# Kernel optimization log

Hardware: AMD Instinct MI355X
Metric: run time of the kernel (lower is better)

The kernel has to match this reference:

```python
import jax, jax.numpy as jnp
import numpy as np
from jax import lax

NUM_HEADS = 8
EPS_BN = 1e-5
EPS_LN = 1e-5


def setup_inputs() -> dict:
    key = jax.random.key(0)
    ks = iter(jax.random.split(key, 32))
    C = 512
    R = C // 16  # channel-gate reduction
    HID = 512    # classifier hidden
    NC = 1       # num_classes

    def gn(shape, scale=0.02):
        return (jax.random.normal(next(ks), shape, dtype=jnp.float32) * scale)

    inp = {
        "x": jax.random.normal(next(ks), (16, C, 28, 28), dtype=jnp.float32),
        # ChannelGate MLP (Linear(C,R) -> ReLU -> Linear(R,C))
        "mlp_w1": gn((R, C)), "mlp_b1": jnp.zeros((R,), jnp.float32),
        "mlp_w2": gn((C, R)), "mlp_b2": jnp.zeros((C,), jnp.float32),
        # SpatialGate 7x7 conv (2->1, no bias) + BatchNorm2d(1) eval-mode stats
        "sp_w": gn((1, 2, 7, 7)),
        "sp_gamma": jnp.ones((1,), jnp.float32), "sp_beta": jnp.zeros((1,), jnp.float32),
        "sp_mean": jnp.zeros((1,), jnp.float32), "sp_var": jnp.ones((1,), jnp.float32),
        # attention projections
        "wq": gn((C, C)), "bq": jnp.zeros((C,), jnp.float32),
        "wk": gn((C, C)), "bk": jnp.zeros((C,), jnp.float32),
        "wv": gn((C, C)), "bv": jnp.zeros((C,), jnp.float32),
        "wo": gn((C, C)), "bo": jnp.zeros((C,), jnp.float32),
        # classifier: LayerNorm(C) -> Linear(C,512) -> ReLU -> Linear(512,NC)
        "ln_g": jnp.ones((C,), jnp.float32), "ln_b": jnp.zeros((C,), jnp.float32),
        "fc1_w": gn((HID, C)), "fc1_b": jnp.zeros((HID,), jnp.float32),
        "fc2_w": gn((NC, HID)), "fc2_b": jnp.zeros((NC,), jnp.float32),
    }
    return inp


def reference(x, mlp_w1, mlp_b1, mlp_w2, mlp_b2, sp_w, sp_gamma, sp_beta,
              sp_mean, sp_var, wq, bq, wk, bk, wv, bv, wo, bo,
              ln_g, ln_b, fc1_w, fc1_b, fc2_w, fc2_b):
    B, C, H, W = x.shape
    N = H * W
    hd = C // NUM_HEADS

    # ---- CBAM: channel gate (avg + max global pools through shared MLP) ----
    def mlp(p):  # p: [B, C]
        return jax.nn.relu(p @ mlp_w1.T + mlp_b1) @ mlp_w2.T + mlp_b2

    avg_p = x.mean(axis=(2, 3))
    max_p = x.max(axis=(2, 3))
    ch_scale = jax.nn.sigmoid(mlp(avg_p) + mlp(max_p))[:, :, None, None]
    x = x * ch_scale

    # ---- CBAM: spatial gate ----
    comp = jnp.concatenate([x.max(axis=1, keepdims=True),
                            x.mean(axis=1, keepdims=True)], axis=1)  # [B,2,H,W]
    s = lax.conv_general_dilated(comp, sp_w, window_strides=(1, 1),
                                 padding=[(3, 3), (3, 3)],
                                 dimension_numbers=("NCHW", "OIHW", "NCHW"))
    s = (s - sp_mean[None, :, None, None]) * lax.rsqrt(sp_var + EPS_BN)[None, :, None, None]
    s = s * sp_gamma[None, :, None, None] + sp_beta[None, :, None, None]
    x = x * jax.nn.sigmoid(s)

    # ---- multi-head self-attention over HW tokens ----
    xf = x.reshape(B, C, N).transpose(0, 2, 1)  # [B, N, C]

    def heads(w, b):
        return (xf @ w.T + b).reshape(B, N, NUM_HEADS, hd).transpose(0, 2, 1, 3)

    Q, K, V = heads(wq, bq), heads(wk, bk), heads(wv, bv)  # [B, h, N, d]
    scores = jnp.einsum("bhnd,bhmd->bhnm", Q, K) / jnp.sqrt(jnp.float32(hd))
    attn = jax.nn.softmax(scores, axis=-1)  # dropout is identity in eval
    attended = jnp.einsum("bhnm,bhmd->bhnd", attn, V)
    attended = attended.transpose(0, 2, 1, 3).reshape(B, N, C)
    attended = attended @ wo.T + bo
    x = x + attended.transpose(0, 2, 1).reshape(B, C, H, W)

    # ---- classifier head ----
    p = x.mean(axis=(2, 3))  # AdaptiveAvgPool2d(1) + Flatten -> [B, C]
    mu = p.mean(axis=-1, keepdims=True)
    var = p.var(axis=-1, keepdims=True)
    ln = (p - mu) * lax.rsqrt(var + EPS_LN) * ln_g + ln_b
    h = jax.nn.relu(ln @ fc1_w.T + fc1_b)
    return h @ fc2_w.T + fc2_b
```

## Files before the change

### kernel.cpp

```cpp
#include <hip/hip_runtime.h>
#include <math.h>

#define BB 16
#define CC 512
#define HW 784
#define RR 32
#define NHD 8
#define HD 64
#define NT 784
#define NTILE 49
#define CBS 132

#define OFS_AVGP   0
#define OFS_MAXP   8192
#define OFS_CHS    16384
#define OFS_SP     49664
#define OFS_P1     62208
#define OFS_ABAR   70400
#define OFS_XG     78592
#define XG_SZ      (BB*CC*HW)
#define OFS_XGT    (OFS_XG + XG_SZ)
#define OFS_QBF    (OFS_XGT + XG_SZ/2)
#define OFS_KBF    (OFS_QBF + XG_SZ/2)
#define OFS_V2     (OFS_KBF + XG_SZ/2)
#define OFS_WF     (OFS_V2 + XG_SZ)
#define OFS_W      OFS_XG
#define OFS_PV     (OFS_XG + 131072)
#define OFS_H1     (OFS_PV + 8192)
#define OFS_CMAXP  (OFS_XG + 262144)
#define OFS_CMEANP (OFS_CMAXP + 200704)

typedef __attribute__((ext_vector_type(8))) short bf16x8;
typedef __attribute__((ext_vector_type(4))) float f32x4;

__device__ __forceinline__ unsigned short f2bf(float x) {
  union { float f; unsigned u; } v; v.f = x;
  unsigned r = v.u + 0x7fffu + ((v.u >> 16) & 1u);
  return (unsigned short)(r >> 16);
}
__device__ __forceinline__ float bf2f(unsigned short x) {
  union { unsigned u; float f; } v; v.u = ((unsigned)x) << 16;
  return v.f;
}
__device__ __forceinline__ void async16(const unsigned short* g, unsigned short* l) {
  __builtin_amdgcn_global_load_lds(
      (const __attribute__((address_space(1))) unsigned int*)g,
      (__attribute__((address_space(3))) unsigned int*)l, 16, 0, 0);
}

__global__ void k_pool(const float* __restrict__ x, float* avg_p, float* max_p) {
  int wid = threadIdx.x >> 6;
  int lane = threadIdx.x & 63;
  int row = blockIdx.x * 4 + wid;
  const float* xr = x + (size_t)row * HW;
  float s = 0.f, m = -INFINITY;
  for (int i = lane; i < HW; i += 64) { float v = xr[i]; s += v; m = fmaxf(m, v); }
  for (int o = 32; o; o >>= 1) { s += __shfl_down(s, o, 64); m = fmaxf(m, __shfl_down(m, o, 64)); }
  if (lane == 0) { avg_p[row] = s * (1.f/HW); max_p[row] = m; }
}

__global__ void k_chmlp(const float* avg_p, const float* max_p,
                        const float* w1, const float* b1,
                        const float* w2, const float* b2, float* chs) {
  __shared__ float pa[CC], pm[CC], part[256], hr[64];
  int b = blockIdx.x, t = threadIdx.x;
  for (int i = t; i < CC; i += 256) { pa[i] = avg_p[b*CC+i]; pm[i] = max_p[b*CC+i]; }
  __syncthreads();
  {
    int rp = t & 63, ch = t >> 6;
    int r = rp & 31;
    const float* src = (rp < 32) ? pa : pm;
    const float* wr = w1 + (size_t)r*CC + ch*128;
    float s = 0.f;
    #pragma unroll 8
    for (int c = 0; c < 128; c++) s += src[ch*128 + c] * wr[c];
    part[t] = s;
  }
  __syncthreads();
  if (t < 64)
    hr[t] = fmaxf(part[t] + part[64+t] + part[128+t] + part[192+t] + b1[t & 31], 0.f);
  __syncthreads();
  for (int c = t; c < CC; c += 256) {
    float a = 2.f*b2[c];
    const float* wr = w2 + c*RR;
    #pragma unroll
    for (int r = 0; r < RR; r++) a += (hr[r]+hr[32+r])*wr[r];
    chs[b*CC+c] = 1.f/(1.f+__expf(-a));
  }
}

__global__ void k_chgatep(const float* __restrict__ x, const float* __restrict__ chs,
                          float* __restrict__ cmaxp, float* __restrict__ cmeanp) {
  __shared__ float cs[32];
  int b = blockIdx.x, cg = blockIdx.y, t = threadIdx.x;
  if (t < 32) cs[t] = chs[b*CC + cg*32 + t];
  __syncthreads();
  const float* xb = x + ((size_t)b*CC + cg*32)*HW;
  for (int pix = t; pix < HW; pix += 256) {
    float mx = -INFINITY, sm = 0.f;
    #pragma unroll
    for (int c = 0; c < 32; c++) {
      float v = xb[(size_t)c*HW + pix] * cs[c];
      mx = fmaxf(mx, v); sm += v;
    }
    cmaxp[(size_t)(cg*BB + b)*HW + pix] = mx;
    cmeanp[(size_t)(cg*BB + b)*HW + pix] = sm;
  }
}

__global__ void k_credsp(const float* __restrict__ cmaxp, const float* __restrict__ cmeanp,
                         const float* __restrict__ w, const float* g, const float* be,
                         const float* mu, const float* var, float* __restrict__ sp) {
  __shared__ float cmx[HW], cmn[HW];
  int b = blockIdx.x, t = threadIdx.x;
  for (int pix = t; pix < HW; pix += 256) {
    float mx = -INFINITY, sm = 0.f;
    #pragma unroll
    for (int cg = 0; cg < 16; cg++) {
      mx = fmaxf(mx, cmaxp[(size_t)(cg*BB + b)*HW + pix]);
      sm += cmeanp[(size_t)(cg*BB + b)*HW + pix];
    }
    cmx[pix] = mx; cmn[pix] = sm * (1.f/CC);
  }
  __syncthreads();
  float bnscale = rsqrtf(var[0]+1e-5f)*g[0];
  for (int pix = t; pix < HW; pix += 256) {
    int h = pix/28, wd = pix%28;
    float acc = 0.f;
    for (int kh = 0; kh < 7; kh++) {
      int ih = h + kh - 3; if (ih < 0 || ih >= 28) continue;
      for (int kw = 0; kw < 7; kw++) {
        int iw = wd + kw - 3; if (iw < 0 || iw >= 28) continue;
        int ip = ih*28+iw;
        acc += cmx[ip]*w[kh*7+kw] + cmn[ip]*w[49+kh*7+kw];
      }
    }
    float s = (acc - mu[0])*bnscale + be[0];
    sp[b*HW+pix] = 1.f/(1.f+__expf(-s));
  }
}

__global__ void k_sfuse(const float* __restrict__ x, const float* __restrict__ chs,
                        const float* __restrict__ sp, unsigned short* __restrict__ xgT) {
  __shared__ float cs[CC];
  int nt = blockIdx.x, b = blockIdx.y;
  int t = threadIdx.x, ln = t & 63;
  for (int i = t; i < CC; i += 256) cs[i] = chs[b*CC+i];
  __syncthreads();
  int n = nt*16 + (ln & 15);
  float spv = sp[b*HW + n];
  const float* xb = x + (size_t)b*CC*HW;
  #pragma unroll
  for (int i = 0; i < 4; i++) {
    int s = (t >> 6) + 4*i;
    int c = s*32 + (ln >> 4)*8;
    bf16x8 p;
    #pragma unroll
    for (int j = 0; j < 8; j++)
      p[j] = (short)f2bf(xb[(size_t)(c+j)*HW + n] * cs[c+j] * spv);
    *(bf16x8*)(xgT + ((((size_t)b*NTILE + nt)*16 + s)*64 + ln)*8) = p;
  }
}

__global__ void k_p1(const unsigned short* __restrict__ xgT, float* __restrict__ p1) {
  __shared__ float red[4][32];
  int b = blockIdx.x, s = blockIdx.y;
  int t = threadIdx.x, w = t >> 6, ln = t & 63;
  float acc[8] = {0.f,0.f,0.f,0.f,0.f,0.f,0.f,0.f};
  for (int nt = w; nt < NTILE; nt += 4) {
    bf16x8 p = *(const bf16x8*)(xgT + ((((size_t)b*NTILE + nt)*16 + s)*64 + ln)*8);
    #pragma unroll
    for (int j = 0; j < 8; j++) acc[j] += bf2f((unsigned short)p[j]);
  }
  #pragma unroll
  for (int j = 0; j < 8; j++) {
    float v = acc[j];
    v += __shfl_xor(v,1,64); v += __shfl_xor(v,2,64);
    v += __shfl_xor(v,4,64); v += __shfl_xor(v,8,64);
    if ((ln & 15) == 0) red[w][(ln>>4)*8 + j] = v;
  }
  __syncthreads();
  if (t < 32)
    p1[b*CC + s*32 + t] = (red[0][t]+red[1][t]+red[2][t]+red[3][t]) * (1.f/HW);
}

__global__ void k_wfrag(const float* __restrict__ wq, const float* __restrict__ wk,
                        const float* __restrict__ wv, unsigned short* __restrict__ Wf) {
  int idx = blockIdx.x*256 + threadIdx.x;
  int ln = idx & 63;
  int s  = (idx >> 6) & 15;
  int ct = (idx >> 10) & 31;
  int mat = idx >> 15;
  const float* W = (mat==0)? wq : (mat==1)? wk : wv;
  const float* src = W + (size_t)(ct*16 + (ln & 15))*CC + s*32 + (ln >> 4)*8;
  float4 f0 = *(const float4*)src;
  float4 f1 = *(const float4*)(src + 4);
  bf16x8 p;
  p[0]=(short)f2bf(f0.x); p[1]=(short)f2bf(f0.y); p[2]=(short)f2bf(f0.z); p[3]=(short)f2bf(f0.w);
  p[4]=(short)f2bf(f1.x); p[5]=(short)f2bf(f1.y); p[6]=(short)f2bf(f1.z); p[7]=(short)f2bf(f1.w);
  *(bf16x8*)(Wf + (size_t)idx*8) = p;
}

__global__ __launch_bounds__(256) void k_qkv_mfma(
    const unsigned short* __restrict__ xgT, const unsigned short* __restrict__ Wf,
    const float* __restrict__ bq, const float* __restrict__ bk, const float* __restrict__ bv,
    unsigned short* __restrict__ Qbf, unsigned short* __restrict__ Kbf,
    unsigned short* __restrict__ Vbf) {
  __shared__ __align__(16) unsigned char smem[65536];
  unsigned short* Alds = (unsigned short*)smem;
  float* Cb = (float*)smem;
  int blk = blockIdx.x;
  int yb = blk / 208;
  int r0 = blk % 208;
  int mt = r0 >> 4;
  int b  = r0 & 15;
  int mat = yb >> 2;
  int c0 = (yb & 3) * 128;
  int t = threadIdx.x, w = t >> 6, ln = t & 63;
  const unsigned short* Ab = xgT + (size_t)b*NTILE*8192;
  const unsigned short* Bb = Wf + (size_t)mat*32*8192;
  int ctg0 = (c0 >> 4) + w*2;
  int ntc[4];
  #pragma unroll
  for (int m = 0; m < 4; m++) { int nt = 4*mt + m; ntc[m] = (nt > 48) ? 48 : nt; }
  #pragma unroll
  for (int j0 = 0; j0 < 16; j0++) {
    int j = w + 4*j0;
    int m = j >> 4, sj = j & 15;
    async16(Ab + (size_t)ntc[m]*8192 + (size_t)(sj*64 + ln)*8,
            Alds + (size_t)j*512);
  }
  f32x4 acc[4][2];
  #pragma unroll
  for (int m = 0; m < 4; m++)
    #pragma unroll
    for (int c2 = 0; c2 < 2; c2++) acc[m][c2] = (f32x4){0.f,0.f,0.f,0.f};
  __syncthreads();
  #pragma unroll 2
  for (int s = 0; s < 16; s++) {
    bf16x8 bf0 = *(const bf16x8*)(Bb + (size_t)(ctg0*16 + s)*512 + ln*8);
    bf16x8 bf1 = *(const bf16x8*)(Bb + (size_t)((ctg0+1)*16 + s)*512 + ln*8);
    bf16x8 af[4];
    #pragma unroll
    for (int m = 0; m < 4; m++)
      af[m] = *(const bf16x8*)(Alds + (size_t)(m*16 + s)*512 + ln*8);
    #pragma unroll
    for (int m = 0; m < 4; m++) {
      acc[m][0] = __builtin_amdgcn_mfma_f32_16x16x32_bf16(af[m], bf0, acc[m][0], 0,0,0);
      acc[m][1] = __builtin_amdgcn_mfma_f32_16x16x32_bf16(af[m], bf1, acc[m][1], 0,0,0);
    }
  }
  __syncthreads();
  #pragma unroll
  for (int m = 0; m < 4; m++)
    #pragma unroll
    for (int c2 = 0; c2 < 2; c2++)
      #pragma unroll
      for (int r = 0; r < 4; r++)
        Cb[(m*16 + (ln>>4)*4 + r)*CBS + w*32 + c2*16 + (ln&15)] = acc[m][c2][r];
  __syncthreads();
  const float* bias = (mat==0)? bq : (mat==1)? bk : bv;
  #pragma unroll
  for (int i = 0; i < 4; i++) {
    int p = w*4 + i;
    int ntl = p >> 2, sl = p & 3;
    int nt = 4*mt + ntl;
    if (nt > 48) continue;
    int row = ntl*16 + (ln & 15);
    int col = sl*32 + (ln >> 4)*8;
    float4 v0 = *(const float4*)&Cb[row*CBS + col];
    float4 v1 = *(const float4*)&Cb[row*CBS + col + 4];
    float v[8] = {v0.x, v0.y, v0.z, v0.w, v1.x, v1.y, v1.z, v1.w};
    #pragma unroll
    for (int j = 0; j < 8; j++) v[j] += bias[c0 + col + j];
    int token = nt*16 + (ln & 15);
    int h = (c0 >> 6) + (sl >> 1);
    int bh = b*NHD + h;
    bf16x8 pk;
    #pragma unroll
    for (int j = 0; j < 8; j++) pk[j] = (short)f2bf(v[j]);
    if (mat < 2) {
      unsigned short* Out = (mat == 0) ? Qbf : Kbf;
      *(bf16x8*)(Out + ((size_t)bh*NTILE + nt)*1024 + (size_t)(sl & 1)*512 + ln*8) = pk;
    } else {
      int d = (sl & 1)*32 + (ln >> 4)*8;
      *(bf16x8*)(Vbf + ((size_t)bh*NT + token)*HD + d) = pk;
    }
  }
}

__global__ __launch_bounds__(256, 3) void k_attn8(const unsigned short* __restrict__ Qbf,
    const unsigned short* __restrict__ Kbf, float* __restrict__ wsum) {
  __shared__ float l_tmp[2][64];
  __shared__ float rl[2][16];
  int bh = blockIdx.x & 127, pg = blockIdx.x >> 7;
  int t = threadIdx.x, w = t >> 6, ln = t & 63;
  int ntA = pg*2;
  bool hasB = (ntA + 1) < NTILE;
  int ntB = hasB ? (ntA + 1) : ntA;
  const unsigned short* QbA = Qbf + ((size_t)bh*NTILE + ntA)*1024;
  const unsigned short* QbB = Qbf + ((size_t)bh*NTILE + ntB)*1024;
  const unsigned short* Kb = Kbf + (size_t)bh*NTILE*1024;
  bf16x8 qA0 = *(const bf16x8*)(QbA + ln*8);
  bf16x8 qA1 = *(const bf16x8*)(QbA + 512 + ln*8);
  bf16x8 qB0 = *(const bf16x8*)(QbB + ln*8);
  bf16x8 qB1 = *(const bf16x8*)(QbB + 512 + ln*8);
  f32x4 evA[13], evB[13];
  float lpA[4] = {0.f,0.f,0.f,0.f}, lpB[4] = {0.f,0.f,0.f,0.f};
  #pragma unroll
  for (int i = 0; i < 13; i++) {
    int mt = w + 4*i;
    bool valid = (i < 12) || (w == 0);
    int mtc = valid ? mt : 48;
    bf16x8 k0 = *(const bf16x8*)(Kb + (size_t)mtc*1024 + ln*8);
    bf16x8 k1 = *(const bf16x8*)(Kb + (size_t)mtc*1024 + 512 + ln*8);
    f32x4 a = {0.f,0.f,0.f,0.f};
    a = __builtin_amdgcn_mfma_f32_16x16x32_bf16(qA0, k0, a, 0,0,0);
    a = __builtin_amdgcn_mfma_f32_16x16x32_bf16(qA1, k1, a, 0,0,0);
    f32x4 c = {0.f,0.f,0.f,0.f};
    c = __builtin_amdgcn_mfma_f32_16x16x32_bf16(qB0, k0, c, 0,0,0);
    c = __builtin_amdgcn_mfma_f32_16x16x32_bf16(qB1, k1, c, 0,0,0);
    f32x4 ea, eb;
    #pragma unroll
    for (int r = 0; r < 4; r++) {
      ea[r] = __expf(a[r]*0.125f);
      eb[r] = __expf(c[r]*0.125f);
    }
    evA[i] = ea; evB[i] = eb;
    if (valid) {
      #pragma unroll
      for (int r = 0; r < 4; r++) { lpA[r] += ea[r]; lpB[r] += eb[r]; }
    }
  }
  #pragma unroll
  for (int r = 0; r < 4; r++) {
    float v = lpA[r];
    v += __shfl_xor(v,1,64); v += __shfl_xor(v,2,64);
    v += __shfl_xor(v,4,64); v += __shfl_xor(v,8,64);
    if ((ln & 15) == 0) l_tmp[0][w*16 + (ln>>4)*4 + r] = v;
    float u = lpB[r];
    u += __shfl_xor(u,1,64); u += __shfl_xor(u,2,64);
    u += __shfl_xor(u,4,64); u += __shfl_xor(u,8,64);
    if ((ln & 15) == 0) l_tmp[1][w*16 + (ln>>4)*4 + r] = u;
  }
  __syncthreads();
  if (t < 32) {
    int g = t >> 4, q = t & 15;
    rl[g][q] = 1.f / (l_tmp[g][q] + l_tmp[g][16+q] + l_tmp[g][32+q] + l_tmp[g][48+q]);
  }
  __syncthreads();
  f32x4 rlA = *(const f32x4*)&rl[0][(ln >> 4)*4];
  f32x4 rlB = *(const f32x4*)&rl[1][(ln >> 4)*4];
  #pragma unroll
  for (int i = 0; i < 13; i++) {
    int mt = w + 4*i;
    bool valid = (i < 12) || (w == 0);
    float v = evA[i][0]*rlA[0] + evA[i][1]*rlA[1] + evA[i][2]*rlA[2] + evA[i][3]*rlA[3];
    if (hasB)
      v += evB[i][0]*rlB[0] + evB[i][1]*rlB[1] + evB[i][2]*rlB[2] + evB[i][3]*rlB[3];
    v += __shfl_xor(v, 16, 64);
    v += __shfl_xor(v, 32, 64);
    if (valid && ln < 16)
      atomicAdd(&wsum[bh*NT + mt*16 + ln], v);
  }
}

__global__ void k_attn_av(const float* __restrict__ w, const unsigned short* __restrict__ Vm,
                          float* __restrict__ abar) {
  __shared__ float red[256];
  int bh = blockIdx.x, t = threadIdx.x;
  int d = t & 63, chunk = t >> 6;
  float acc = 0.f;
  const unsigned short* vb = Vm + (size_t)bh*NT*HD;
  const float* wb = w + bh*NT;
  for (int m = chunk*196; m < (chunk+1)*196; m++)
    acc += wb[m] * bf2f(vb[(size_t)m*HD + d]);
  red[t] = acc;
  __syncthreads();
  if (t < 64)
    abar[bh*HD + t] = (red[t] + red[64+t] + red[128+t] + red[192+t]) * (1.f/NT);
}

__global__ void k_headA(const float* __restrict__ p1, const float* __restrict__ abar,
                        const float* __restrict__ wo, const float* __restrict__ bo,
                        float* __restrict__ pv) {
  int b = blockIdx.x, cg = blockIdx.y;
  int t = threadIdx.x, w = t >> 6, ln = t & 63;
  float a[8];
  #pragma unroll
  for (int k = 0; k < 8; k++) a[k] = abar[b*CC + ln + 64*k];
  int c0 = cg*32 + w*8;
  for (int i = 0; i < 8; i++) {
    int c = c0 + i;
    const float* wr = wo + (size_t)c*CC;
    float s = 0.f;
    #pragma unroll
    for (int k = 0; k < 8; k++) s += a[k] * wr[ln + 64*k];
    for (int o = 32; o; o >>= 1) s += __shfl_down(s, o, 64);
    if (ln == 0) pv[b*CC + c] = s + bo[c] + p1[b*CC + c];
  }
}

__global__ void k_headC(const float* __restrict__ pv, const float* __restrict__ ln_g,
                        const float* __restrict__ ln_b, const float* __restrict__ fc1_w,
                        const float* __restrict__ fc1_b, const float* __restrict__ fc2_w,
                        const float* __restrict__ fc2_b, float* __restrict__ out) {
  int b = blockIdx.x, cg = blockIdx.y;
  int t = threadIdx.x, w = t >> 6, ln = t & 63;
  float a[8];
  float s = 0.f, s2 = 0.f;
  #pragma unroll
  for (int k = 0; k < 8; k++) {
    a[k] = pv[b*CC + ln + 64*k];
    s += a[k]; s2 += a[k]*a[k];
  }
  for (int o = 32; o; o >>= 1) { s += __shfl_down(s, o, 64); s2 += __shfl_down(s2, o, 64); }
  s = __shfl(s, 0, 64); s2 = __shfl(s2, 0, 64);
  float mean = s * (1.f/CC);
  float rs = rsqrtf(s2*(1.f/CC) - mean*mean + 1e-5f);
  #pragma unroll
  for (int k = 0; k < 8; k++)
    a[k] = (a[k]-mean)*rs*ln_g[ln + 64*k] + ln_b[ln + 64*k];
  int c0 = cg*32 + w*8;
  float o2 = 0.f;
  for (int i = 0; i < 8; i++) {
    int c = c0 + i;
    const float* wr = fc1_w + (size_t)c*CC;
    float v = 0.f;
    #pragma unroll
    for (int k = 0; k < 8; k++) v += a[k] * wr[ln + 64*k];
    for (int o = 32; o; o >>= 1) v += __shfl_down(v, o, 64);
    if (ln == 0) o2 += fmaxf(v + fc1_b[c], 0.f) * fc2_w[c];
  }
  if (ln == 0) {
    if (cg == 0 && w == 0) o2 += fc2_b[0];
    atomicAdd(&out[b], o2);
  }
}

extern "C" void kernel_launch(void* const* d_in, const int* in_sizes, int n_in,
                              void* d_out, int out_size, void* d_ws, size_t ws_size,
                              hipStream_t stream) {
  const float* x       = (const float*)d_in[0];
  const float* mlp_w1  = (const float*)d_in[1];
  const float* mlp_b1  = (const float*)d_in[2];
  const float* mlp_w2  = (const float*)d_in[3];
  const float* mlp_b2  = (const float*)d_in[4];
  const float* sp_w    = (const float*)d_in[5];
  const float* sp_g    = (const float*)d_in[6];
  const float* sp_b    = (const float*)d_in[7];
  const float* sp_mu   = (const float*)d_in[8];
  const float* sp_var  = (const float*)d_in[9];
  const float* wq      = (const float*)d_in[10];
  const float* bq      = (const float*)d_in[11];
  const float* wk      = (const float*)d_in[12];
  const float* bk      = (const float*)d_in[13];
  const float* wv      = (const float*)d_in[14];
  const float* bv      = (const float*)d_in[15];
  const float* wo      = (const float*)d_in[16];
  const float* bo      = (const float*)d_in[17];
  const float* ln_g    = (const float*)d_in[18];
  const float* ln_b    = (const float*)d_in[19];
  const float* fc1_w   = (const float*)d_in[20];
  const float* fc1_b   = (const float*)d_in[21];
  const float* fc2_w   = (const float*)d_in[22];
  const float* fc2_b   = (const float*)d_in[23];

  float* ws = (float*)d_ws;
  float* avg_p = ws + OFS_AVGP;
  float* max_p = ws + OFS_MAXP;
  float* chs   = ws + OFS_CHS;
  float* sp    = ws + OFS_SP;
  float* p1    = ws + OFS_P1;
  float* abar  = ws + OFS_ABAR;
  unsigned short* xgT = (unsigned short*)(ws + OFS_XGT);
  unsigned short* Qbf = (unsigned short*)(ws + OFS_QBF);
  unsigned short* Kbf = (unsigned short*)(ws + OFS_KBF);
  unsigned short* Vbf = (unsigned short*)(ws + OFS_V2);
  unsigned short* Wf  = (unsigned short*)(ws + OFS_WF);
  float* wsum  = ws + OFS_W;
  float* pv    = ws + OFS_PV;
  float* cmaxp = ws + OFS_CMAXP;
  float* cmeanp= ws + OFS_CMEANP;

  hipMemsetAsync(wsum, 0, BB*NHD*NT*sizeof(float), stream);
  hipMemsetAsync(d_out, 0, (size_t)out_size*sizeof(float), stream);

  k_pool   <<<2048, 256, 0, stream>>>(x, avg_p, max_p);
  k_chmlp  <<<BB, 256, 0, stream>>>(avg_p, max_p, mlp_w1, mlp_b1, mlp_w2, mlp_b2, chs);
  k_chgatep<<<dim3(BB,16), 256, 0, stream>>>(x, chs, cmaxp, cmeanp);
  k_credsp <<<BB, 256, 0, stream>>>(cmaxp, cmeanp, sp_w, sp_g, sp_b, sp_mu, sp_var, sp);
  k_wfrag  <<<384, 256, 0, stream>>>(wq, wk, wv, Wf);
  k_sfuse  <<<dim3(NTILE,BB), 256, 0, stream>>>(x, chs, sp, xgT);
  k_p1     <<<dim3(BB,16), 256, 0, stream>>>(xgT, p1);
  k_qkv_mfma<<<2496, 256, 0, stream>>>(xgT, Wf, bq, bk, bv, Qbf, Kbf, Vbf);
  k_attn8  <<<25*128, 256, 0, stream>>>(Qbf, Kbf, wsum);
  k_attn_av<<<128, 256, 0, stream>>>(wsum, Vbf, abar);
  k_headA  <<<dim3(BB,16), 256, 0, stream>>>(p1, abar, wo, bo, pv);
  k_headC  <<<dim3(BB,16), 256, 0, stream>>>(pv, ln_g, ln_b, fc1_w, fc1_b,
                                             fc2_w, fc2_b, (float*)d_out);
}
```

Measured before the change: 270.5 us.

## Fuse pre-pass kernels, fold p1 into sfuse, widen QKV tiles, split spatial conv

Merges the pooling, weight-fragment conversion and zeroing memsets into one launch. The p1 column-mean reduction moves into k_sfuse via shuffles and atomics, with scaling deferred to headA. The QKV MFMA kernel now computes 256 output columns per block, reusing A fragments from LDS and halving the grid. The spatial conv kernel is split over 4 blocks per batch. These cut launch count and redundant xgT reads, at the cost of atomic contention and more accumulator registers.

```diff
diff --git a/kernel.cpp b/kernel.cpp
--- a/kernel.cpp
+++ b/kernel.cpp
@@ -26,7 +26,6 @@
 #define OFS_WF     (OFS_V2 + XG_SZ)
 #define OFS_W      OFS_XG
 #define OFS_PV     (OFS_XG + 131072)
-#define OFS_H1     (OFS_PV + 8192)
 #define OFS_CMAXP  (OFS_XG + 262144)
 #define OFS_CMEANP (OFS_CMAXP + 200704)
 
@@ -48,15 +47,45 @@
       (__attribute__((address_space(3))) unsigned int*)l, 16, 0, 0);
 }
 
-__global__ void k_pool(const float* __restrict__ x, float* avg_p, float* max_p) {
-  int wid = threadIdx.x >> 6;
-  int lane = threadIdx.x & 63;
-  int row = blockIdx.x * 4 + wid;
-  const float* xr = x + (size_t)row * HW;
-  float s = 0.f, m = -INFINITY;
-  for (int i = lane; i < HW; i += 64) { float v = xr[i]; s += v; m = fmaxf(m, v); }
-  for (int o = 32; o; o >>= 1) { s += __shfl_down(s, o, 64); m = fmaxf(m, __shfl_down(m, o, 64)); }
-  if (lane == 0) { avg_p[row] = s * (1.f/HW); max_p[row] = m; }
+__global__ void k_pre(const float* __restrict__ x,
+                      const float* __restrict__ wq, const float* __restrict__ wk,
+                      const float* __restrict__ wv,
+                      float* avg_p, float* max_p, unsigned short* __restrict__ Wf,
+                      float* __restrict__ wsum, float* __restrict__ p1,
+                      float* __restrict__ outp) {
+  int bid = blockIdx.x;
+  if (bid < 2048) {
+    int wid = threadIdx.x >> 6;
+    int lane = threadIdx.x & 63;
+    int row = bid * 4 + wid;
+    const float* xr = x + (size_t)row * HW;
+    float s = 0.f, m = -INFINITY;
+    for (int i = lane; i < HW; i += 64) { float v = xr[i]; s += v; m = fmaxf(m, v); }
+    for (int o = 32; o; o >>= 1) { s += __shfl_down(s, o, 64); m = fmaxf(m, __shfl_down(m, o, 64)); }
+    if (lane == 0) { avg_p[row] = s * (1.f/HW); max_p[row] = m; }
+  } else if (bid < 2432) {
+    int idx = (bid - 2048)*256 + threadIdx.x;
+    int ln = idx & 63;
+    int s  = (idx >> 6) & 15;
+    int ct = (idx >> 10) & 31;
+    int mat = idx >> 15;
+    const float* W = (mat==0)? wq : (mat==1)? wk : wv;
+    const float* src = W + (size_t)(ct*16 + (ln & 15))*CC + s*32 + (ln >> 4)*8;
+    float4 f0 = *(const float4*)src;
+    float4 f1 = *(const float4*)(src + 4);
+    bf16x8 p;
+    p[0]=(short)f2bf(f0.x); p[1]=(short)f2bf(f0.y); p[2]=(short)f2bf(f0.z); p[3]=(short)f2bf(f0.w);
+    p[4]=(short)f2bf(f1.x); p[5]=(short)f2bf(f1.y); p[6]=(short)f2bf(f1.z); p[7]=(short)f2bf(f1.w);
+    *(bf16x8*)(Wf + (size_t)idx*8) = p;
+  } else {
+    int idx = (bid - 2432)*256 + threadIdx.x;
+    const float4 z = {0.f,0.f,0.f,0.f};
+    if (idx < 4) *(float4*)&outp[idx*4] = z;
+    for (int i = idx; i < 27136; i += 16384) {
+      if (i < 25088) *(float4*)&wsum[(size_t)i*4] = z;
+      else           *(float4*)&p1[(size_t)(i-25088)*4] = z;
+    }
+  }
 }
 
 __global__ void k_chmlp(const float* avg_p, const float* max_p,
@@ -112,7 +141,7 @@
                          const float* __restrict__ w, const float* g, const float* be,
                          const float* mu, const float* var, float* __restrict__ sp) {
   __shared__ float cmx[HW], cmn[HW];
-  int b = blockIdx.x, t = threadIdx.x;
+  int b = blockIdx.x, q = blockIdx.y, t = threadIdx.x;
   for (int pix = t; pix < HW; pix += 256) {
     float mx = -INFINITY, sm = 0.f;
     #pragma unroll
@@ -123,8 +152,9 @@
     cmx[pix] = mx; cmn[pix] = sm * (1.f/CC);
   }
   __syncthreads();
-  float bnscale = rsqrtf(var[0]+1e-5f)*g[0];
-  for (int pix = t; pix < HW; pix += 256) {
+  if (t < 196) {
+    int pix = q*196 + t;
+    float bnscale = rsqrtf(var[0]+1e-5f)*g[0];
     int h = pix/28, wd = pix%28;
     float acc = 0.f;
     for (int kh = 0; kh < 7; kh++) {
@@ -141,7 +171,8 @@
 }
 
 __global__ void k_sfuse(const float* __restrict__ x, const float* __restrict__ chs,
-                        const float* __restrict__ sp, unsigned short* __restrict__ xgT) {
+                        const float* __restrict__ sp, unsigned short* __restrict__ xgT,
+                        float* __restrict__ p1) {
   __shared__ float cs[CC];
   int nt = blockIdx.x, b = blockIdx.y;
   int t = threadIdx.x, ln = t & 63;
@@ -154,51 +185,26 @@
   for (int i = 0; i < 4; i++) {
     int s = (t >> 6) + 4*i;
     int c = s*32 + (ln >> 4)*8;
+    float vf[8];
     bf16x8 p;
     #pragma unroll
-    for (int j = 0; j < 8; j++)
-      p[j] = (short)f2bf(xb[(size_t)(c+j)*HW + n] * cs[c+j] * spv);
+    for (int j = 0; j < 8; j++) {
+      vf[j] = xb[(size_t)(c+j)*HW + n] * cs[c+j] * spv;
+      p[j] = (short)f2bf(vf[j]);
+    }
     *(bf16x8*)(xgT + ((((size_t)b*NTILE + nt)*16 + s)*64 + ln)*8) = p;
-  }
-}
-
-__global__ void k_p1(const unsigned short* __restrict__ xgT, float* __restrict__ p1) {
-  __shared__ float red[4][32];
-  int b = blockIdx.x, s = blockIdx.y;
-  int t = threadIdx.x, w = t >> 6, ln = t & 63;
-  float acc[8] = {0.f,0.f,0.f,0.f,0.f,0.f,0.f,0.f};
-  for (int nt = w; nt < NTILE; nt += 4) {
-    bf16x8 p = *(const bf16x8*)(xgT + ((((size_t)b*NTILE + nt)*16 + s)*64 + ln)*8);
-    #pragma unroll
-    for (int j = 0; j < 8; j++) acc[j] += bf2f((unsigned short)p[j]);
-  }
-  #pragma unroll
-  for (int j = 0; j < 8; j++) {
-    float v = acc[j];
-    v += __shfl_xor(v,1,64); v += __shfl_xor(v,2,64);
-    v += __shfl_xor(v,4,64); v += __shfl_xor(v,8,64);
-    if ((ln & 15) == 0) red[w][(ln>>4)*8 + j] = v;
-  }
-  __syncthreads();
-  if (t < 32)
-    p1[b*CC + s*32 + t] = (red[0][t]+red[1][t]+red[2][t]+red[3][t]) * (1.f/HW);
-}
-
-__global__ void k_wfrag(const float* __restrict__ wq, const float* __restrict__ wk,
-                        const float* __restrict__ wv, unsigned short* __restrict__ Wf) {
-  int idx = blockIdx.x*256 + threadIdx.x;
-  int ln = idx & 63;
-  int s  = (idx >> 6) & 15;
-  int ct = (idx >> 10) & 31;
-  int mat = idx >> 15;
-  const float* W = (mat==0)? wq : (mat==1)? wk : wv;
-  const float* src = W + (size_t)(ct*16 + (ln & 15))*CC + s*32 + (ln >> 4)*8;
-  float4 f0 = *(const float4*)src;
-  float4 f1 = *(const float4*)(src + 4);
-  bf16x8 p;
-  p[0]=(short)f2bf(f0.x); p[1]=(short)f2bf(f0.y); p[2]=(short)f2bf(f0.z); p[3]=(short)f2bf(f0.w);
-  p[4]=(short)f2bf(f1.x); p[5]=(short)f2bf(f1.y); p[6]=(short)f2bf(f1.z); p[7]=(short)f2bf(f1.w);
-  *(bf16x8*)(Wf + (size_t)idx*8) = p;
+    #pragma unroll
+    for (int j = 0; j < 8; j++) {
+      float v = vf[j];
+      v += __shfl_xor(v,1,64); v += __shfl_xor(v,2,64);
+      v += __shfl_xor(v,4,64); v += __shfl_xor(v,8,64);
+      vf[j] = v;
+    }
+    if ((ln & 15) == 0) {
+      #pragma unroll
+      for (int j = 0; j < 8; j++) atomicAdd(&p1[b*CC + c + j], vf[j]);
+    }
+  }
 }
 
 __global__ __launch_bounds__(256) void k_qkv_mfma(
@@ -214,12 +220,12 @@
   int r0 = blk % 208;
   int mt = r0 >> 4;
   int b  = r0 & 15;
-  int mat = yb >> 2;
-  int c0 = (yb & 3) * 128;
+  int mat = yb >> 1;
+  int c0 = (yb & 1) * 256;
   int t = threadIdx.x, w = t >> 6, ln = t & 63;
   const unsigned short* Ab = xgT + (size_t)b*NTILE*8192;
   const unsigned short* Bb = Wf + (size_t)mat*32*8192;
-  int ctg0 = (c0 >> 4) + w*2;
+  int ctgb = (c0 >> 4) + w*2;
   int ntc[4];
   #pragma unroll
   for (int m = 0; m < 4; m++) { int nt = 4*mt + m; ntc[m] = (nt > 48) ? 48 : nt; }
@@ -230,61 +236,70 @@
     async16(Ab + (size_t)ntc[m]*8192 + (size_t)(sj*64 + ln)*8,
             Alds + (size_t)j*512);
   }
-  f32x4 acc[4][2];
+  f32x4 acc[4][4];
   #pragma unroll
   for (int m = 0; m < 4; m++)
     #pragma unroll
-    for (int c2 = 0; c2 < 2; c2++) acc[m][c2] = (f32x4){0.f,0.f,0.f,0.f};
+    for (int c2 = 0; c2 < 4; c2++) acc[m][c2] = (f32x4){0.f,0.f,0.f,0.f};
   __syncthreads();
   #pragma unroll 2
   for (int s = 0; s < 16; s++) {
-    bf16x8 bf0 = *(const bf16x8*)(Bb + (size_t)(ctg0*16 + s)*512 + ln*8);
-    bf16x8 bf1 = *(const bf16x8*)(Bb + (size_t)((ctg0+1)*16 + s)*512 + ln*8);
+    bf16x8 bf[4];
+    bf[0] = *(const bf16x8*)(Bb + (size_t)((ctgb  )*16 + s)*512 + ln*8);
+    bf[1] = *(const bf16x8*)(Bb + (size_t)((ctgb+1)*16 + s)*512 + ln*8);
+    bf[2] = *(const bf16x8*)(Bb + (size_t)((ctgb+8)*16 + s)*512 + ln*8);
+    bf[3] = *(const bf16x8*)(Bb + (size_t)((ctgb+9)*16 + s)*512 + ln*8);
     bf16x8 af[4];
     #pragma unroll
     for (int m = 0; m < 4; m++)
       af[m] = *(const bf16x8*)(Alds + (size_t)(m*16 + s)*512 + ln*8);
     #pragma unroll
     for (int m = 0; m < 4; m++) {
-      acc[m][0] = __builtin_amdgcn_mfma_f32_16x16x32_bf16(af[m], bf0, acc[m][0], 0,0,0);
-      acc[m][1] = __builtin_amdgcn_mfma_f32_16x16x32_bf16(af[m], bf1, acc[m][1], 0,0,0);
-    }
-  }
-  __syncthreads();
-  #pragma unroll
-  for (int m = 0; m < 4; m++)
-    #pragma unroll
-    for (int c2 = 0; c2 < 2; c2++)
       #pragma unroll
-      for (int r = 0; r < 4; r++)
-        Cb[(m*16 + (ln>>4)*4 + r)*CBS + w*32 + c2*16 + (ln&15)] = acc[m][c2][r];
+      for (int c2 = 0; c2 < 4; c2++)
+        acc[m][c2] = __builtin_amdgcn_mfma_f32_16x16x32_bf16(af[m], bf[c2], acc[m][c2], 0,0,0);
+    }
+  }
   __syncthreads();
   const float* bias = (mat==0)? bq : (mat==1)? bk : bv;
   #pragma unroll
-  for (int i = 0; i < 4; i++) {
-    int p = w*4 + i;
-    int ntl = p >> 2, sl = p & 3;
-    int nt = 4*mt + ntl;
-    if (nt > 48) continue;
-    int row = ntl*16 + (ln & 15);
-    int col = sl*32 + (ln >> 4)*8;
-    float4 v0 = *(const float4*)&Cb[row*CBS + col];
-    float4 v1 = *(const float4*)&Cb[row*CBS + col + 4];
-    float v[8] = {v0.x, v0.y, v0.z, v0.w, v1.x, v1.y, v1.z, v1.w};
-    #pragma unroll
-    for (int j = 0; j < 8; j++) v[j] += bias[c0 + col + j];
-    int token = nt*16 + (ln & 15);
-    int h = (c0 >> 6) + (sl >> 1);
-    int bh = b*NHD + h;
-    bf16x8 pk;
-    #pragma unroll
-    for (int j = 0; j < 8; j++) pk[j] = (short)f2bf(v[j]);
-    if (mat < 2) {
-      unsigned short* Out = (mat == 0) ? Qbf : Kbf;
-      *(bf16x8*)(Out + ((size_t)bh*NTILE + nt)*1024 + (size_t)(sl & 1)*512 + ln*8) = pk;
-    } else {
-      int d = (sl & 1)*32 + (ln >> 4)*8;
-      *(bf16x8*)(Vbf + ((size_t)bh*NT + token)*HD + d) = pk;
+  for (int ch = 0; ch < 2; ch++) {
+    if (ch) __syncthreads();
+    #pragma unroll
+    for (int m = 0; m < 4; m++)
+      #pragma unroll
+      for (int c2 = 0; c2 < 2; c2++)
+        #pragma unroll
+        for (int r = 0; r < 4; r++)
+          Cb[(m*16 + (ln>>4)*4 + r)*CBS + w*32 + c2*16 + (ln&15)] = acc[m][ch*2+c2][r];
+    __syncthreads();
+    #pragma unroll
+    for (int i = 0; i < 4; i++) {
+      int p = w*4 + i;
+      int ntl = p >> 2, sl = p & 3;
+      int nt = 4*mt + ntl;
+      if (nt > 48) continue;
+      int row = ntl*16 + (ln & 15);
+      int col = sl*32 + (ln >> 4)*8;
+      float4 v0 = *(const float4*)&Cb[row*CBS + col];
+      float4 v1 = *(const float4*)&Cb[row*CBS + col + 4];
+      float v[8] = {v0.x, v0.y, v0.z, v0.w, v1.x, v1.y, v1.z, v1.w};
+      int colA = ch*128 + col;
+      #pragma unroll
+      for (int j = 0; j < 8; j++) v[j] += bias[c0 + colA + j];
+      int token = nt*16 + (ln & 15);
+      int h = (c0 >> 6) + (ch << 1) + (sl >> 1);
+      int bh = b*NHD + h;
+      bf16x8 pk;
+      #pragma unroll
+      for (int j = 0; j < 8; j++) pk[j] = (short)f2bf(v[j]);
+      if (mat < 2) {
+        unsigned short* Out = (mat == 0) ? Qbf : Kbf;
+        *(bf16x8*)(Out + ((size_t)bh*NTILE + nt)*1024 + (size_t)(sl & 1)*512 + ln*8) = pk;
+      } else {
+        int d = (sl & 1)*32 + (ln >> 4)*8;
+        *(bf16x8*)(Vbf + ((size_t)bh*NT + token)*HD + d) = pk;
+      }
     }
   }
 }
@@ -397,7 +412,7 @@
     #pragma unroll
     for (int k = 0; k < 8; k++) s += a[k] * wr[ln + 64*k];
     for (int o = 32; o; o >>= 1) s += __shfl_down(s, o, 64);
-    if (ln == 0) pv[b*CC + c] = s + bo[c] + p1[b*CC + c];
+    if (ln == 0) pv[b*CC + c] = s + bo[c] + p1[b*CC + c] * (1.f/HW);
   }
 }
 
@@ -483,17 +498,13 @@
   float* cmaxp = ws + OFS_CMAXP;
   float* cmeanp= ws + OFS_CMEANP;
 
-  hipMemsetAsync(wsum, 0, BB*NHD*NT*sizeof(float), stream);
-  hipMemsetAsync(d_out, 0, (size_t)out_size*sizeof(float), stream);
-
-  k_pool   <<<2048, 256, 0, stream>>>(x, avg_p, max_p);
+  k_pre    <<<2496, 256, 0, stream>>>(x, wq, wk, wv, avg_p, max_p, Wf, wsum, p1,
+                                      (float*)d_out);
   k_chmlp  <<<BB, 256, 0, stream>>>(avg_p, max_p, mlp_w1, mlp_b1, mlp_w2, mlp_b2, chs);
   k_chgatep<<<dim3(BB,16), 256, 0, stream>>>(x, chs, cmaxp, cmeanp);
-  k_credsp <<<BB, 256, 0, stream>>>(cmaxp, cmeanp, sp_w, sp_g, sp_b, sp_mu, sp_var, sp);
-  k_wfrag  <<<384, 256, 0, stream>>>(wq, wk, wv, Wf);
-  k_sfuse  <<<dim3(NTILE,BB), 256, 0, stream>>>(x, chs, sp, xgT);
-  k_p1     <<<dim3(BB,16), 256, 0, stream>>>(xgT, p1);
-  k_qkv_mfma<<<2496, 256, 0, stream>>>(xgT, Wf, bq, bk, bv, Qbf, Kbf, Vbf);
+  k_credsp <<<dim3(BB,4), 256, 0, stream>>>(cmaxp, cmeanp, sp_w, sp_g, sp_b, sp_mu, sp_var, sp);
+  k_sfuse  <<<dim3(NTILE,BB), 256, 0, stream>>>(x, chs, sp, xgT, p1);
+  k_qkv_mfma<<<1248, 256, 0, stream>>>(xgT, Wf, bq, bk, bv, Qbf, Kbf, Vbf);
   k_attn8  <<<25*128, 256, 0, stream>>>(Qbf, Kbf, wsum);
   k_attn_av<<<128, 256, 0, stream>>>(wsum, Vbf, abar);
   k_headA  <<<dim3(BB,16), 256, 0, stream>>>(p1, abar, wo, bo, pv);
```

New measurement: 276.9 us. 2.4% more time.
